# Optimization experiments

Measured on AMD Instinct MI355X. Metric: run time of the kernel, lower is better.

## Reference

```python
import jax, jax.numpy as jnp
import numpy as np

U, I, E = 50000, 100000, 1600000
D, H, HID, B = 64, 8, 8, 16384
ALPHA = 0.2  # leaky relu slope


def setup_inputs() -> dict:
    key = jax.random.key(0)
    ks = jax.random.split(key, 12)
    return {
        "userIdx": jax.random.randint(ks[0], (B,), 0, U),
        "itemIdx": jax.random.randint(ks[1], (B,), 0, I),
        "edge_u": jax.random.randint(ks[2], (E,), 0, U),
        "edge_i": jax.random.randint(ks[3], (E,), 0, I),
        "uEmbd": jax.random.normal(ks[4], (U, D), dtype=jnp.float32) * 0.01,
        "iEmbd": jax.random.normal(ks[5], (I, D), dtype=jnp.float32) * 0.01,
        "Wu_h": jax.random.normal(ks[6], (H, D, HID), dtype=jnp.float32) * 0.18,
        "Wi_h": jax.random.normal(ks[7], (H, D, HID), dtype=jnp.float32) * 0.18,
        "a_h": jax.random.normal(ks[8], (H, 2 * HID), dtype=jnp.float32) * 0.3,
        "Wu_out": jax.random.normal(ks[9], (H * HID, D), dtype=jnp.float32) * 0.15,
        "Wi_out": jax.random.normal(ks[10], (H * HID, D), dtype=jnp.float32) * 0.15,
        "a_out": jax.random.normal(ks[11], (2 * D,), dtype=jnp.float32) * 0.1,
    }


def _leaky(x):
    return jnp.where(x >= 0, x, ALPHA * x)


def _gat_layer(fu, fi, Wu, Wi, a, edge_u, edge_i):
    # fu:[U,in], fi:[I,in], Wu/Wi:[in,out], a:[2*out]
    u_h = fu @ Wu  # [U,out]
    i_h = fi @ Wi  # [I,out]
    out = Wu.shape[1]
    # a . cat(u_h[eu], i_h[ei]) decomposed into per-node scores then edge gather
    su = u_h @ a[:out]  # [U]
    si = i_h @ a[out:]  # [I]
    e = jnp.exp(-_leaky(su[edge_u] + si[edge_i]))  # [E]
    rowsum = jax.ops.segment_sum(e, edge_u, num_segments=U)  # [U]
    colsum = jax.ops.segment_sum(e, edge_i, num_segments=I)  # [I]
    # users aggregate items they interacted with
    agg_i = jax.ops.segment_sum(e[:, None] * i_h[edge_i], edge_u, num_segments=U)  # [U,out]
    u_p = u_h + agg_i / jnp.where(rowsum == 0, 1.0, rowsum)[:, None]
    # items aggregate users (nan from empty cols -> 0, as in original)
    agg_u = jax.ops.segment_sum(e[:, None] * u_h[edge_u], edge_i, num_segments=I)  # [I,out]
    att_u = jnp.where((colsum > 0)[:, None], agg_u / jnp.where(colsum == 0, 1.0, colsum)[:, None], 0.0)
    i_p = i_h + att_u
    return u_p, i_p


def reference(userIdx, itemIdx, edge_u, edge_i, uEmbd, iEmbd, Wu_h, Wi_h, a_h, Wu_out, Wi_out, a_out):
    # eval mode: all dropout layers are identity
    fu, fi = uEmbd, iEmbd
    head = jax.vmap(lambda Wu, Wi, a: _gat_layer(fu, fi, Wu, Wi, a, edge_u, edge_i))
    u_ps, i_ps = head(Wu_h, Wi_h, a_h)  # [H,U,HID], [H,I,HID]
    # concat=True heads: elu then concatenate along feature dim (head-major columns)
    hu = jax.nn.elu(u_ps).transpose(1, 0, 2).reshape(U, H * HID)
    hi = jax.nn.elu(i_ps).transpose(1, 0, 2).reshape(I, H * HID)
    u_p, i_p = _gat_layer(hu, hi, Wu_out, Wi_out, a_out, edge_u, edge_i)
    u_f = jax.nn.elu(u_p)  # final F.elu in SpUIGAT
    i_f = jax.nn.elu(i_p)
    return jnp.sum(u_f[userIdx] * i_f[itemIdx], axis=1)  # [B]
```

## Files before the change

kernel.cpp:

```cpp
#include <hip/hip_runtime.h>
#include <hip/hip_fp16.h>

#define U_N 50000
#define I_N 100000
#define E_N 1600000
#define B_N 16384
#define UI_N (U_N + I_N)
#define NB_U 782
#define NB_I 1563
#define NBK 586
#define CAP 10240
#define NBLD 512
#define CHUNK (E_N / NBLD)
#define COL_CAP 3300000
#define MAXACT 32768
#define FP8_SCALE 128.0f

typedef float f32x2 __attribute__((ext_vector_type(2)));

__global__ __launch_bounds__(1024) void k_build1(
    const int* __restrict__ eu, const int* __restrict__ ei,
    int* __restrict__ bcnt, int* __restrict__ storage) {
  __shared__ int hist[NBK];
  __shared__ int lbase[NBK];
  __shared__ int loff[NBK];
  int t = threadIdx.x;
  for (int b = t; b < NBK; b += 1024) { hist[b] = 0; loff[b] = 0; }
  __syncthreads();
  int e0 = blockIdx.x * CHUNK;
  int myu[4], myi[4];
  int ne = 0;
#pragma unroll
  for (int k = 0; k < 4; k++) {
    int e = e0 + t + 1024 * k;
    if (e < e0 + CHUNK) {
      int u = eu[e], it = ei[e];
      myu[k] = u;
      myi[k] = it;
      ne = k + 1;
      atomicAdd(&hist[u >> 8], 1);
      atomicAdd(&hist[(U_N + it) >> 8], 1);
    }
  }
  __syncthreads();
  for (int b = t; b < NBK; b += 1024) {
    int h = hist[b];
    lbase[b] = h ? atomicAdd(&bcnt[b], h) : 0;
  }
  __syncthreads();
#pragma unroll
  for (int k = 0; k < 4; k++) {
    if (k < ne) {
      int u = myu[k], it = myi[k];
      int k2 = U_N + it;
      int b1 = u >> 8;
      int s1 = lbase[b1] + atomicAdd(&loff[b1], 1);
      storage[(size_t)b1 * CAP + s1] = ((u & 255) << 18) | k2;
      int b2 = k2 >> 8;
      int s2 = lbase[b2] + atomicAdd(&loff[b2], 1);
      storage[(size_t)b2 * CAP + s2] = ((k2 & 255) << 18) | u;
    }
  }
}

__device__ void build2_body(int b, const int* __restrict__ bcnt,
                            const int* __restrict__ storage,
                            int* __restrict__ ptr, int* __restrict__ col,
                            int* smem) {
  int* c = smem;
  int* sc = smem + 256;
  int* pb = smem + 512;
  int* cur = smem + 768;
  int t = threadIdx.x;
  int pre = 0;
  for (int i = t; i < b; i += 256) pre += bcnt[i];
  sc[t] = pre;
  c[t] = 0;
  __syncthreads();
  for (int o = 128; o > 0; o >>= 1) {
    if (t < o) sc[t] += sc[t + o];
    __syncthreads();
  }
  int base = sc[0];
  __syncthreads();
  int n = bcnt[b];
  const int* s = storage + (size_t)b * CAP;
  for (int i = t; i < n; i += 256) atomicAdd(&c[s[i] >> 18], 1);
  __syncthreads();
  int deg = c[t];
  sc[t] = deg;
  __syncthreads();
  int val = deg;
  for (int o = 1; o < 256; o <<= 1) {
    int x = (t >= o) ? sc[t - o] : 0;
    __syncthreads();
    val += x;
    sc[t] = val;
    __syncthreads();
  }
  int myPtr = base + (val - deg);
  pb[t] = myPtr;
  cur[t] = 0;
  int node = b * 256 + t;
  if (node < UI_N) ptr[node] = myPtr;
  if (b == NBK - 1 && t == 255) ptr[UI_N] = base + val;
  __syncthreads();
  for (int i = t; i < n; i += 256) {
    int e = s[i];
    int local = e >> 18;
    int slot = pb[local] + atomicAdd(&cur[local], 1);
    col[slot] = e & 0x3FFFF;
  }
}

__device__ __forceinline__ void flagc_body(int bid, const int* __restrict__ uIdx,
                                           const int* __restrict__ iIdx,
                                           int* __restrict__ flag, int* __restrict__ list,
                                           int* __restrict__ nm) {
  int b = bid * 256 + threadIdx.x;
  if (b < B_N) {
    int u = uIdx[b];
    if (atomicExch(&flag[u], 1) == 0) list[atomicAdd(nm, 1)] = u;
    int it = U_N + iIdx[b];
    if (atomicExch(&flag[it], 1) == 0) list[atomicAdd(nm, 1)] = it;
  }
}

__device__ __forceinline__ void mm2_body(
    int bid, const float* __restrict__ Xu32, const float* __restrict__ Xi32,
    const __half* __restrict__ X16,
    const float* __restrict__ Wu, const float* __restrict__ Wi,
    const float* __restrict__ a, int layer,
    __half* __restrict__ f16,
    unsigned char* __restrict__ f8,
    __half* __restrict__ s16,
    float* Wl, float* Xs) {
  const bool isU = bid < NB_U;
  const int N = isU ? U_N : I_N;
  const int base = (isU ? bid : bid - NB_U) * 64;
  const int gofs = isU ? 0 : U_N;
  const float* W = isU ? Wu : Wi;
  const int aoff = (layer == 1) ? (isU ? 0 : 8) : (isU ? 0 : 64);
  int t = threadIdx.x;

  if (layer == 1) {
#pragma unroll
    for (int k = 0; k < 4; k++) {
      int i = t + 256 * k;
      int h = i >> 7, d = (i >> 1) & 63, half = i & 1;
      float4 v = *(const float4*)(W + h * 512 + d * 8 + half * 4);
      *(float4*)(Wl + d * 64 + h * 8 + half * 4) = v;
    }
    const float* X = isU ? Xu32 : Xi32;
#pragma unroll
    for (int k = 0; k < 4; k++) {
      int i = t + 256 * k;
      int r = i >> 4, ch = i & 15;
      int node = base + r;
      float4 v = make_float4(0.f, 0.f, 0.f, 0.f);
      if (node < N) v = *(const float4*)(X + (size_t)node * 64 + ch * 4);
      *(float4*)(Xs + r * 64 + ch * 4) = v;
    }
  } else {
#pragma unroll
    for (int k = 0; k < 4; k++) {
      int i = t + 256 * k;
      *(float4*)(Wl + i * 4) = *(const float4*)(W + i * 4);
    }
#pragma unroll
    for (int k = 0; k < 4; k++) {
      int i = t + 256 * k;
      int r = i >> 4, ch = i & 15;
      int node = base + r;
      float4 v = make_float4(0.f, 0.f, 0.f, 0.f);
      if (node < N) {
        const __half2* hp = (const __half2*)(X16 + (size_t)(gofs + node) * 64 + ch * 4);
        float2 f0 = __half22float2(hp[0]);
        float2 f1 = __half22float2(hp[1]);
        v = make_float4(f0.x, f0.y, f1.x, f1.y);
      }
      *(float4*)(Xs + r * 64 + ch * 4) = v;
    }
  }
  __syncthreads();

  const int c0 = t & 31;
  const int rb = t >> 5;
  float acc0[8], acc1[8];
#pragma unroll
  for (int k = 0; k < 8; k++) { acc0[k] = 0.f; acc1[k] = 0.f; }

  for (int d0 = 0; d0 < 64; d0 += 4) {
    float2 wA = *(float2*)(Wl + (d0 + 0) * 64 + 2 * c0);
    float2 wB = *(float2*)(Wl + (d0 + 1) * 64 + 2 * c0);
    float2 wC = *(float2*)(Wl + (d0 + 2) * 64 + 2 * c0);
    float2 wD = *(float2*)(Wl + (d0 + 3) * 64 + 2 * c0);
#pragma unroll
    for (int k = 0; k < 8; k++) {
      float4 x = *(float4*)(Xs + (rb + 8 * k) * 64 + d0);
      acc0[k] += x.x * wA.x + x.y * wB.x + x.z * wC.x + x.w * wD.x;
      acc1[k] += x.x * wA.y + x.y * wB.y + x.z * wC.y + x.w * wD.y;
    }
  }

  float av0, av1;
  if (layer == 1) {
    int h = c0 >> 2, j = 2 * (c0 & 3);
    av0 = a[h * 16 + aoff + j];
    av1 = a[h * 16 + aoff + j + 1];
  } else {
    av0 = a[aoff + 2 * c0];
    av1 = a[aoff + 2 * c0 + 1];
  }
#pragma unroll
  for (int k = 0; k < 8; k++) {
    int node = base + rb + 8 * k;
    float s = acc0[k] * av0 + acc1[k] * av1;
    s += __shfl_xor(s, 1);
    s += __shfl_xor(s, 2);
    if (layer != 1) {
      s += __shfl_xor(s, 4);
      s += __shfl_xor(s, 8);
      s += __shfl_xor(s, 16);
    }
    if (node < N) {
      int gn = gofs + node;
      float2 f;
      f.x = acc0[k];
      f.y = acc1[k];
      *(__half2*)(f16 + (size_t)gn * 64 + 2 * c0) = __float22half2_rn(f);
      int pk = __builtin_amdgcn_cvt_pk_fp8_f32(acc0[k] * FP8_SCALE,
                                               acc1[k] * FP8_SCALE, 0, false);
      *(unsigned short*)(f8 + (size_t)gn * 64 + 2 * c0) = (unsigned short)pk;
      if (layer == 1) {
        if ((c0 & 3) == 0) s16[gn * 8 + (c0 >> 2)] = __float2half_rn(s);
      } else {
        if (c0 == 0) s16[gn] = __float2half_rn(s);
      }
    }
  }
}

__global__ __launch_bounds__(256) void k_fused2(
    const int* __restrict__ bcnt, const int* __restrict__ storage,
    int* __restrict__ ptr, int* __restrict__ col,
    const int* __restrict__ uIdx, const int* __restrict__ iIdx,
    int* __restrict__ flag, int* __restrict__ list, int* __restrict__ nm,
    const float* __restrict__ uEmbd, const float* __restrict__ iEmbd,
    const float* __restrict__ Wu, const float* __restrict__ Wi,
    const float* __restrict__ a, __half* __restrict__ fA,
    unsigned char* __restrict__ fA8, __half* __restrict__ s16) {
  __shared__ float4 smv[2048];
  int bx = blockIdx.x;
  if (bx < NBK) {
    build2_body(bx, bcnt, storage, ptr, col, (int*)smv);
  } else if (bx < NBK + 64) {
    flagc_body(bx - NBK, uIdx, iIdx, flag, list, nm);
  } else {
    float* s = (float*)smv;
    mm2_body(bx - NBK - 64, uEmbd, iEmbd, nullptr, Wu, Wi, a, 1, fA, fA8, s16,
             s, s + 4096);
  }
}

__global__ __launch_bounds__(256) void k_mm2(
    const __half* __restrict__ X16, const float* __restrict__ Wu,
    const float* __restrict__ Wi, const float* __restrict__ a,
    __half* __restrict__ f16, unsigned char* __restrict__ f8,
    __half* __restrict__ s2) {
  __shared__ float4 smv[2048];
  float* s = (float*)smv;
  mm2_body(blockIdx.x, nullptr, nullptr, X16, Wu, Wi, a, 2, f16, f8, s2, s, s + 4096);
}

template <int LAYER>
__device__ __forceinline__ void agg_body(
    const int* __restrict__ ptr, const int* __restrict__ col,
    const unsigned char* __restrict__ f8,
    const __half* __restrict__ fA,
    __half* __restrict__ fB,
    const __half* __restrict__ sc,
    const int* __restrict__ list, const int* __restrict__ nm) {
  int gid = blockIdx.x * blockDim.x + threadIdx.x;
  int wv = gid >> 6;
  int l = threadIdx.x & 63;
  int half = l >> 5;
  int idx = wv * 2 + half;
  bool act = true;
  int n;
  if (LAYER == 2) {
    act = idx < *nm;
    n = act ? list[idx] : 0;
  } else {
    n = idx;
  }
  int lh = l & 31;
  int g = lh >> 3;
  int cc = lh & 7;

  int beg = ptr[n], endA = ptr[n + 1];
  int deg = act ? (endA - beg) : 0;
  unsigned coff = ((unsigned)(beg + g)) << 2;
  const unsigned begb = (unsigned)beg << 2;
  const unsigned f8sh = (unsigned)cc << 3;
  const unsigned ssh = (LAYER == 1) ? ((unsigned)cc << 1) : 0u;
  float sself = (LAYER == 1) ? __half2float(sc[(size_t)n * 8 + cc])
                             : __half2float(sc[n]);
  f32x2 acc2[4];
#pragma unroll
  for (int k = 0; k < 4; k++) acc2[k] = (f32x2){0.f, 0.f};
  float wsum = 0.f;
  const char* colc = (const char*)col;
  const char* f8c = (const char*)f8;
  const char* scc = (const char*)sc;

  auto edge = [&](unsigned off) {
    int nb = *(const int*)(colc + off);
    unsigned so = (LAYER == 1) ? (((unsigned)nb << 4) + ssh) : ((unsigned)nb << 1);
    float x = sself + __half2float(*(const __half*)(scc + so));
    int2 r = *(const int2*)(f8c + (((unsigned)nb << 6) + f8sh));
    float w = __expf(-fmaxf(x, 0.2f * x));
    wsum += w;
    f32x2 w2 = {w, w};
    acc2[0] += w2 * __builtin_amdgcn_cvt_pk_f32_fp8((unsigned)r.x, false);
    acc2[1] += w2 * __builtin_amdgcn_cvt_pk_f32_fp8((unsigned)r.x, true);
    acc2[2] += w2 * __builtin_amdgcn_cvt_pk_f32_fp8((unsigned)r.y, false);
    acc2[3] += w2 * __builtin_amdgcn_cvt_pk_f32_fp8((unsigned)r.y, true);
  };
  auto edgem = [&](unsigned off, bool valid) {
    unsigned o = valid ? off : begb;
    int nb = *(const int*)(colc + o);
    unsigned so = (LAYER == 1) ? (((unsigned)nb << 4) + ssh) : ((unsigned)nb << 1);
    float x = sself + __half2float(*(const __half*)(scc + so));
    int2 r = *(const int2*)(f8c + (((unsigned)nb << 6) + f8sh));
    float w = valid ? __expf(-fmaxf(x, 0.2f * x)) : 0.f;
    wsum += w;
    f32x2 w2 = {w, w};
    acc2[0] += w2 * __builtin_amdgcn_cvt_pk_f32_fp8((unsigned)r.x, false);
    acc2[1] += w2 * __builtin_amdgcn_cvt_pk_f32_fp8((unsigned)r.x, true);
    acc2[2] += w2 * __builtin_amdgcn_cvt_pk_f32_fp8((unsigned)r.y, false);
    acc2[3] += w2 * __builtin_amdgcn_cvt_pk_f32_fp8((unsigned)r.y, true);
  };

  int q = deg >> 4;
  for (; q > 0; q--) {
    edge(coff);
    edge(coff + 16);
    edge(coff + 32);
    edge(coff + 48);
    coff += 64;
  }
  int rem = deg & 15;
  if (rem) {
    edgem(coff, g < rem);
    edgem(coff + 16, (4 + g) < rem);
    if (rem > 8) {
      edgem(coff + 32, (8 + g) < rem);
      edgem(coff + 48, (12 + g) < rem);
    }
  }

#pragma unroll
  for (int k = 0; k < 4; k++) {
    f32x2 t;
    t.x = __shfl_xor(acc2[k].x, 8);
    t.y = __shfl_xor(acc2[k].y, 8);
    acc2[k] += t;
    t.x = __shfl_xor(acc2[k].x, 16);
    t.y = __shfl_xor(acc2[k].y, 16);
    acc2[k] += t;
  }
  wsum += __shfl_xor(wsum, 8);
  wsum += __shfl_xor(wsum, 16);

  if (act) {
    float inv = (deg > 0) ? 1.f / (wsum * FP8_SCALE) : 0.f;
    f32x2 a2;
    if (g == 0) a2 = acc2[0];
    else if (g == 1) a2 = acc2[1];
    else if (g == 2) a2 = acc2[2];
    else a2 = acc2[3];
    size_t boff = (size_t)n * 64 + cc * 8 + 2 * g;
    float2 sf = __half22float2(*(const __half2*)(fA + boff));
    float v0 = sf.x + a2.x * inv;
    float v1 = sf.y + a2.y * inv;
    v0 = (v0 > 0.f) ? v0 : (__expf(v0) - 1.f);
    v1 = (v1 > 0.f) ? v1 : (__expf(v1) - 1.f);
    *(__half2*)(fB + boff) = __floats2half2_rn(v0, v1);
  }
}

__global__ __launch_bounds__(256) void k_aggL1(
    const int* __restrict__ ptr, const int* __restrict__ col,
    const unsigned char* __restrict__ f8, const __half* __restrict__ fA,
    __half* __restrict__ fB, const __half* __restrict__ s16) {
  agg_body<1>(ptr, col, f8, fA, fB, s16, nullptr, nullptr);
}

__global__ __launch_bounds__(256) void k_aggL2(
    const int* __restrict__ ptr, const int* __restrict__ col,
    const unsigned char* __restrict__ f8, const __half* __restrict__ fA,
    __half* __restrict__ fB, const __half* __restrict__ s2,
    const int* __restrict__ list, const int* __restrict__ nm) {
  agg_body<2>(ptr, col, f8, fA, fB, s2, list, nm);
}

__global__ void k_dot(const int* __restrict__ uIdx, const int* __restrict__ iIdx,
                      const __half* __restrict__ u_f, const __half* __restrict__ i_f,
                      float* __restrict__ out) {
  int t = threadIdx.x;
  int pair = blockIdx.x * 32 + (t >> 3);
  int cc = t & 7;
  float4 ra = *(const float4*)(u_f + (size_t)uIdx[pair] * 64 + cc * 8);
  float4 rb = *(const float4*)(i_f + (size_t)iIdx[pair] * 64 + cc * 8);
  const __half* ha = (const __half*)&ra;
  const __half* hb = (const __half*)&rb;
  float v = 0.f;
#pragma unroll
  for (int k = 0; k < 8; k++) v += (float)ha[k] * (float)hb[k];
  v += __shfl_xor(v, 1);
  v += __shfl_xor(v, 2);
  v += __shfl_xor(v, 4);
  if (cc == 0) out[pair] = v;
}

extern "C" void kernel_launch(void* const* d_in, const int* in_sizes, int n_in,
                              void* d_out, int out_size, void* d_ws, size_t ws_size,
                              hipStream_t stream) {
  const int* userIdx = (const int*)d_in[0];
  const int* itemIdx = (const int*)d_in[1];
  const int* edge_u = (const int*)d_in[2];
  const int* edge_i = (const int*)d_in[3];
  const float* uEmbd = (const float*)d_in[4];
  const float* iEmbd = (const float*)d_in[5];
  const float* Wu_h = (const float*)d_in[6];
  const float* Wi_h = (const float*)d_in[7];
  const float* a_h = (const float*)d_in[8];
  const float* Wu_out = (const float*)d_in[9];
  const float* Wi_out = (const float*)d_in[10];
  const float* a_out = (const float*)d_in[11];
  float* out = (float*)d_out;

  char* w = (char*)d_ws;
  size_t off = 0;
  auto alloc = [&](size_t bytes) -> void* {
    void* p = w + off;
    off += (bytes + 511) & ~(size_t)511;
    return p;
  };
  int* bcnt = (int*)alloc((size_t)(NBK + 16 + UI_N) * 4);
  int* nm = bcnt + NBK;
  int* flag = bcnt + NBK + 16;
  int* ptr = (int*)alloc((size_t)(UI_N + 1) * 4);
  int* list = (int*)alloc((size_t)MAXACT * 4);
  int* col = (int*)alloc((size_t)COL_CAP * 4);
  __half* fA = (__half*)alloc((size_t)UI_N * 64 * 2);
  unsigned char* fA8 = (unsigned char*)alloc((size_t)UI_N * 64);
  __half* s16 = (__half*)alloc((size_t)UI_N * 8 * 2);
  __half* s2 = (__half*)alloc((size_t)UI_N * 2);
  size_t union_off = off;
  int* storage = (int*)alloc((size_t)NBK * CAP * 4);
  size_t end_storage = off;
  off = union_off;
  __half* fB = (__half*)alloc((size_t)UI_N * 64 * 2);
  if (off < end_storage) off = end_storage;

  hipMemsetAsync(bcnt, 0, (size_t)(NBK + 16 + UI_N) * 4, stream);
  k_build1<<<NBLD, 1024, 0, stream>>>(edge_u, edge_i, bcnt, storage);

  k_fused2<<<NBK + 64 + NB_U + NB_I, 256, 0, stream>>>(
      bcnt, storage, ptr, col, userIdx, itemIdx, flag, list, nm,
      uEmbd, iEmbd, Wu_h, Wi_h, a_h, fA, fA8, s16);

  k_aggL1<<<UI_N * 32 / 256, 256, 0, stream>>>(ptr, col, fA8, fA, fB, s16);

  k_mm2<<<NB_U + NB_I, 256, 0, stream>>>(fB, Wu_out, Wi_out, a_out, fA, fA8, s2);
  k_aggL2<<<MAXACT * 32 / 256, 256, 0, stream>>>(ptr, col, fA8, fA, fB, s2, list, nm);

  k_dot<<<B_N / 32, 256, 0, stream>>>(userIdx, itemIdx, fB, fB + (size_t)U_N * 64, out);
}
```

Before: 275.7 us.

## Stage CSR build through shared memory and skip unneeded layer-2 fp16 writes

The first build pass now counting-sorts each block's edges into LDS with 16-aligned bucket segments, then writes them to global storage in coalesced runs padded with -1. This replaces scattered per-edge global stores. The second pass skips the padding, scatters columns into LDS, and copies them out coalesced using separate true edge counts. Layer-2 matmul only writes fp16 features for flagged (queried) nodes, which cuts write traffic. The cost is larger LDS footprints that lower occupancy, fewer build blocks, and a bigger per-bucket capacity.

```diff
diff --git a/kernel.cpp b/kernel.cpp
--- a/kernel.cpp
+++ b/kernel.cpp
@@ -9,8 +9,8 @@
 #define NB_U 782
 #define NB_I 1563
 #define NBK 586
-#define CAP 10240
-#define NBLD 512
+#define CAP 16384
+#define NBLD 256
 #define CHUNK (E_N / NBLD)
 #define COL_CAP 3300000
 #define MAXACT 32768
@@ -20,60 +20,87 @@
 
 __global__ __launch_bounds__(1024) void k_build1(
     const int* __restrict__ eu, const int* __restrict__ ei,
-    int* __restrict__ bcnt, int* __restrict__ storage) {
+    int* __restrict__ bcnt, int* __restrict__ ecnt, int* __restrict__ storage) {
   __shared__ int hist[NBK];
-  __shared__ int lbase[NBK];
+  __shared__ int pb16[NBK];
+  __shared__ int gbase[NBK];
   __shared__ int loff[NBK];
+  __shared__ short map16[1344];
+  __shared__ int sc[1024];
+  __shared__ int sorted[21504];
   int t = threadIdx.x;
   for (int b = t; b < NBK; b += 1024) { hist[b] = 0; loff[b] = 0; }
   __syncthreads();
   int e0 = blockIdx.x * CHUNK;
-  int myu[4], myi[4];
-  int ne = 0;
-#pragma unroll
-  for (int k = 0; k < 4; k++) {
-    int e = e0 + t + 1024 * k;
-    if (e < e0 + CHUNK) {
+  int myu[7], myi[7];
+#pragma unroll
+  for (int k = 0; k < 7; k++) {
+    myu[k] = -1;
+    if (t + 1024 * k < CHUNK) {
+      int e = e0 + t + 1024 * k;
       int u = eu[e], it = ei[e];
       myu[k] = u;
       myi[k] = it;
-      ne = k + 1;
       atomicAdd(&hist[u >> 8], 1);
       atomicAdd(&hist[(U_N + it) >> 8], 1);
     }
   }
   __syncthreads();
-  for (int b = t; b < NBK; b += 1024) {
-    int h = hist[b];
-    lbase[b] = h ? atomicAdd(&bcnt[b], h) : 0;
-  }
-  __syncthreads();
-#pragma unroll
-  for (int k = 0; k < 4; k++) {
-    if (k < ne) {
+  int ph = (t < NBK) ? ((hist[t] + 15) & ~15) : 0;
+  sc[t] = ph;
+  __syncthreads();
+  int val = ph;
+  for (int o = 1; o < 1024; o <<= 1) {
+    int x = (t >= o) ? sc[t - o] : 0;
+    __syncthreads();
+    val += x;
+    sc[t] = val;
+    __syncthreads();
+  }
+  int total16 = sc[1023];
+  if (t < NBK) {
+    int myb = val - ph;
+    pb16[t] = myb;
+    gbase[t] = ph ? atomicAdd(&bcnt[t], ph) : 0;
+    if (hist[t]) atomicAdd(&ecnt[t], hist[t]);
+    for (int k = myb >> 4; k < (myb + ph) >> 4; k++) map16[k] = (short)t;
+  }
+  for (int j = t; j < total16; j += 1024) sorted[j] = -1;
+  __syncthreads();
+#pragma unroll
+  for (int k = 0; k < 7; k++) {
+    if (myu[k] >= 0) {
       int u = myu[k], it = myi[k];
       int k2 = U_N + it;
       int b1 = u >> 8;
-      int s1 = lbase[b1] + atomicAdd(&loff[b1], 1);
-      storage[(size_t)b1 * CAP + s1] = ((u & 255) << 18) | k2;
+      int p1 = pb16[b1] + atomicAdd(&loff[b1], 1);
+      sorted[p1] = ((u & 255) << 18) | k2;
       int b2 = k2 >> 8;
-      int s2 = lbase[b2] + atomicAdd(&loff[b2], 1);
-      storage[(size_t)b2 * CAP + s2] = ((k2 & 255) << 18) | u;
-    }
+      int p2 = pb16[b2] + atomicAdd(&loff[b2], 1);
+      sorted[p2] = ((k2 & 255) << 18) | u;
+    }
+  }
+  __syncthreads();
+  for (int j = t; j < total16; j += 1024) {
+    int b = map16[j >> 4];
+    storage[(size_t)b * CAP + gbase[b] + (j - pb16[b])] = sorted[j];
   }
 }
 
 __device__ void build2_body(int b, const int* __restrict__ bcnt,
+                            const int* __restrict__ ecnt,
                             const int* __restrict__ storage,
                             int* __restrict__ ptr, int* __restrict__ col,
                             int* smem) {
   int* c = smem;
   int* sc = smem + 256;
-  int* pb = smem + 512;
+  int* pbl = smem + 512;
   int* cur = smem + 768;
+  int* tot = smem + 1024;
+  int* lcol = smem + 1040;
   int t = threadIdx.x;
   int pre = 0;
-  for (int i = t; i < b; i += 256) pre += bcnt[i];
+  for (int i = t; i < b; i += 256) pre += ecnt[i];
   sc[t] = pre;
   c[t] = 0;
   __syncthreads();
@@ -85,7 +112,10 @@
   __syncthreads();
   int n = bcnt[b];
   const int* s = storage + (size_t)b * CAP;
-  for (int i = t; i < n; i += 256) atomicAdd(&c[s[i] >> 18], 1);
+  for (int i = t; i < n; i += 256) {
+    int e = s[i];
+    if (e >= 0) atomicAdd(&c[e >> 18], 1);
+  }
   __syncthreads();
   int deg = c[t];
   sc[t] = deg;
@@ -98,19 +128,25 @@
     sc[t] = val;
     __syncthreads();
   }
-  int myPtr = base + (val - deg);
-  pb[t] = myPtr;
+  int myoff = val - deg;
+  pbl[t] = myoff;
   cur[t] = 0;
+  if (t == 255) tot[0] = val;
   int node = b * 256 + t;
-  if (node < UI_N) ptr[node] = myPtr;
+  if (node < UI_N) ptr[node] = base + myoff;
   if (b == NBK - 1 && t == 255) ptr[UI_N] = base + val;
   __syncthreads();
   for (int i = t; i < n; i += 256) {
     int e = s[i];
-    int local = e >> 18;
-    int slot = pb[local] + atomicAdd(&cur[local], 1);
-    col[slot] = e & 0x3FFFF;
-  }
+    if (e >= 0) {
+      int local = e >> 18;
+      int pos = pbl[local] + atomicAdd(&cur[local], 1);
+      lcol[pos] = e & 0x3FFFF;
+    }
+  }
+  __syncthreads();
+  int vt = tot[0];
+  for (int i = t; i < vt; i += 256) col[base + i] = lcol[i];
 }
 
 __device__ __forceinline__ void flagc_body(int bid, const int* __restrict__ uIdx,
@@ -131,9 +167,8 @@
     const __half* __restrict__ X16,
     const float* __restrict__ Wu, const float* __restrict__ Wi,
     const float* __restrict__ a, int layer,
-    __half* __restrict__ f16,
-    unsigned char* __restrict__ f8,
-    __half* __restrict__ s16,
+    __half* __restrict__ f16, unsigned char* __restrict__ f8,
+    __half* __restrict__ s16, const int* __restrict__ flagp,
     float* Wl, float* Xs) {
   const bool isU = bid < NB_U;
   const int N = isU ? U_N : I_N;
@@ -225,10 +260,12 @@
     }
     if (node < N) {
       int gn = gofs + node;
-      float2 f;
-      f.x = acc0[k];
-      f.y = acc1[k];
-      *(__half2*)(f16 + (size_t)gn * 64 + 2 * c0) = __float22half2_rn(f);
+      if (layer == 1 || flagp[gn]) {
+        float2 f;
+        f.x = acc0[k];
+        f.y = acc1[k];
+        *(__half2*)(f16 + (size_t)gn * 64 + 2 * c0) = __float22half2_rn(f);
+      }
       int pk = __builtin_amdgcn_cvt_pk_fp8_f32(acc0[k] * FP8_SCALE,
                                                acc1[k] * FP8_SCALE, 0, false);
       *(unsigned short*)(f8 + (size_t)gn * 64 + 2 * c0) = (unsigned short)pk;
@@ -242,7 +279,8 @@
 }
 
 __global__ __launch_bounds__(256) void k_fused2(
-    const int* __restrict__ bcnt, const int* __restrict__ storage,
+    const int* __restrict__ bcnt, const int* __restrict__ ecnt,
+    const int* __restrict__ storage,
     int* __restrict__ ptr, int* __restrict__ col,
     const int* __restrict__ uIdx, const int* __restrict__ iIdx,
     int* __restrict__ flag, int* __restrict__ list, int* __restrict__ nm,
@@ -250,16 +288,16 @@
     const float* __restrict__ Wu, const float* __restrict__ Wi,
     const float* __restrict__ a, __half* __restrict__ fA,
     unsigned char* __restrict__ fA8, __half* __restrict__ s16) {
-  __shared__ float4 smv[2048];
+  __shared__ __align__(16) int smem_i[11296];
   int bx = blockIdx.x;
   if (bx < NBK) {
-    build2_body(bx, bcnt, storage, ptr, col, (int*)smv);
+    build2_body(bx, bcnt, ecnt, storage, ptr, col, smem_i);
   } else if (bx < NBK + 64) {
     flagc_body(bx - NBK, uIdx, iIdx, flag, list, nm);
   } else {
-    float* s = (float*)smv;
+    float* s = (float*)smem_i;
     mm2_body(bx - NBK - 64, uEmbd, iEmbd, nullptr, Wu, Wi, a, 1, fA, fA8, s16,
-             s, s + 4096);
+             nullptr, s, s + 4096);
   }
 }
 
@@ -267,10 +305,10 @@
     const __half* __restrict__ X16, const float* __restrict__ Wu,
     const float* __restrict__ Wi, const float* __restrict__ a,
     __half* __restrict__ f16, unsigned char* __restrict__ f8,
-    __half* __restrict__ s2) {
-  __shared__ float4 smv[2048];
-  float* s = (float*)smv;
-  mm2_body(blockIdx.x, nullptr, nullptr, X16, Wu, Wi, a, 2, f16, f8, s2, s, s + 4096);
+    __half* __restrict__ s2, const int* __restrict__ flag) {
+  __shared__ __align__(16) float smv[8192];
+  mm2_body(blockIdx.x, nullptr, nullptr, X16, Wu, Wi, a, 2, f16, f8, s2, flag,
+           smv, smv + 4096);
 }
 
 template <int LAYER>
@@ -448,9 +486,10 @@
     off += (bytes + 511) & ~(size_t)511;
     return p;
   };
-  int* bcnt = (int*)alloc((size_t)(NBK + 16 + UI_N) * 4);
-  int* nm = bcnt + NBK;
-  int* flag = bcnt + NBK + 16;
+  int* bcnt = (int*)alloc((size_t)(2 * NBK + 16 + UI_N) * 4);
+  int* ecnt = bcnt + NBK;
+  int* nm = bcnt + 2 * NBK;
+  int* flag = bcnt + 2 * NBK + 16;
   int* ptr = (int*)alloc((size_t)(UI_N + 1) * 4);
   int* list = (int*)alloc((size_t)MAXACT * 4);
   int* col = (int*)alloc((size_t)COL_CAP * 4);
@@ -465,16 +504,16 @@
   __half* fB = (__half*)alloc((size_t)UI_N * 64 * 2);
   if (off < end_storage) off = end_storage;
 
-  hipMemsetAsync(bcnt, 0, (size_t)(NBK + 16 + UI_N) * 4, stream);
-  k_build1<<<NBLD, 1024, 0, stream>>>(edge_u, edge_i, bcnt, storage);
+  hipMemsetAsync(bcnt, 0, (size_t)(2 * NBK + 16 + UI_N) * 4, stream);
+  k_build1<<<NBLD, 1024, 0, stream>>>(edge_u, edge_i, bcnt, ecnt, storage);
 
   k_fused2<<<NBK + 64 + NB_U + NB_I, 256, 0, stream>>>(
-      bcnt, storage, ptr, col, userIdx, itemIdx, flag, list, nm,
+      bcnt, ecnt, storage, ptr, col, userIdx, itemIdx, flag, list, nm,
       uEmbd, iEmbd, Wu_h, Wi_h, a_h, fA, fA8, s16);
 
   k_aggL1<<<UI_N * 32 / 256, 256, 0, stream>>>(ptr, col, fA8, fA, fB, s16);
 
-  k_mm2<<<NB_U + NB_I, 256, 0, stream>>>(fB, Wu_out, Wi_out, a_out, fA, fA8, s2);
+  k_mm2<<<NB_U + NB_I, 256, 0, stream>>>(fB, Wu_out, Wi_out, a_out, fA, fA8, s2, flag);
   k_aggL2<<<MAXACT * 32 / 256, 256, 0, stream>>>(ptr, col, fA8, fA, fB, s2, list, nm);
 
   k_dot<<<B_N / 32, 256, 0, stream>>>(userIdx, itemIdx, fB, fB + (size_t)U_N * 64, out);
```

Result: no change. 270.4 us (-1.9%).

## Replace bucketed CSR build with global degree count, scan, and atomic scatter

Applied to the files above, without the earlier changes.

The two-pass bucket-storage CSR build is replaced by three steps: a per-node degree count with global atomics, a per-256-node prefix-scan kernel, and a scatter that claims slots with global atomicAdd cursors. The scatter runs in the same launch as the layer-1 projection. This drops the large intermediate storage buffer and its extra read and write pass, but adds an extra kernel launch and heavy global atomic contention on per-node counters. Two smaller changes ride along: attention scores are pre-multiplied by log2(e) so the edge weight uses exp2f instead of __expf, and layer 2 writes fp16 features only for flagged nodes.

```diff
diff --git a/kernel.cpp b/kernel.cpp
--- a/kernel.cpp
+++ b/kernel.cpp
@@ -9,109 +9,14 @@
 #define NB_U 782
 #define NB_I 1563
 #define NBK 586
-#define CAP 10240
-#define NBLD 512
-#define CHUNK (E_N / NBLD)
+#define NCB 2000
+#define ECB 800
 #define COL_CAP 3300000
 #define MAXACT 32768
 #define FP8_SCALE 128.0f
+#define LOG2E 1.44269504088896f
 
 typedef float f32x2 __attribute__((ext_vector_type(2)));
-
-__global__ __launch_bounds__(1024) void k_build1(
-    const int* __restrict__ eu, const int* __restrict__ ei,
-    int* __restrict__ bcnt, int* __restrict__ storage) {
-  __shared__ int hist[NBK];
-  __shared__ int lbase[NBK];
-  __shared__ int loff[NBK];
-  int t = threadIdx.x;
-  for (int b = t; b < NBK; b += 1024) { hist[b] = 0; loff[b] = 0; }
-  __syncthreads();
-  int e0 = blockIdx.x * CHUNK;
-  int myu[4], myi[4];
-  int ne = 0;
-#pragma unroll
-  for (int k = 0; k < 4; k++) {
-    int e = e0 + t + 1024 * k;
-    if (e < e0 + CHUNK) {
-      int u = eu[e], it = ei[e];
-      myu[k] = u;
-      myi[k] = it;
-      ne = k + 1;
-      atomicAdd(&hist[u >> 8], 1);
-      atomicAdd(&hist[(U_N + it) >> 8], 1);
-    }
-  }
-  __syncthreads();
-  for (int b = t; b < NBK; b += 1024) {
-    int h = hist[b];
-    lbase[b] = h ? atomicAdd(&bcnt[b], h) : 0;
-  }
-  __syncthreads();
-#pragma unroll
-  for (int k = 0; k < 4; k++) {
-    if (k < ne) {
-      int u = myu[k], it = myi[k];
-      int k2 = U_N + it;
-      int b1 = u >> 8;
-      int s1 = lbase[b1] + atomicAdd(&loff[b1], 1);
-      storage[(size_t)b1 * CAP + s1] = ((u & 255) << 18) | k2;
-      int b2 = k2 >> 8;
-      int s2 = lbase[b2] + atomicAdd(&loff[b2], 1);
-      storage[(size_t)b2 * CAP + s2] = ((k2 & 255) << 18) | u;
-    }
-  }
-}
-
-__device__ void build2_body(int b, const int* __restrict__ bcnt,
-                            const int* __restrict__ storage,
-                            int* __restrict__ ptr, int* __restrict__ col,
-                            int* smem) {
-  int* c = smem;
-  int* sc = smem + 256;
-  int* pb = smem + 512;
-  int* cur = smem + 768;
-  int t = threadIdx.x;
-  int pre = 0;
-  for (int i = t; i < b; i += 256) pre += bcnt[i];
-  sc[t] = pre;
-  c[t] = 0;
-  __syncthreads();
-  for (int o = 128; o > 0; o >>= 1) {
-    if (t < o) sc[t] += sc[t + o];
-    __syncthreads();
-  }
-  int base = sc[0];
-  __syncthreads();
-  int n = bcnt[b];
-  const int* s = storage + (size_t)b * CAP;
-  for (int i = t; i < n; i += 256) atomicAdd(&c[s[i] >> 18], 1);
-  __syncthreads();
-  int deg = c[t];
-  sc[t] = deg;
-  __syncthreads();
-  int val = deg;
-  for (int o = 1; o < 256; o <<= 1) {
-    int x = (t >= o) ? sc[t - o] : 0;
-    __syncthreads();
-    val += x;
-    sc[t] = val;
-    __syncthreads();
-  }
-  int myPtr = base + (val - deg);
-  pb[t] = myPtr;
-  cur[t] = 0;
-  int node = b * 256 + t;
-  if (node < UI_N) ptr[node] = myPtr;
-  if (b == NBK - 1 && t == 255) ptr[UI_N] = base + val;
-  __syncthreads();
-  for (int i = t; i < n; i += 256) {
-    int e = s[i];
-    int local = e >> 18;
-    int slot = pb[local] + atomicAdd(&cur[local], 1);
-    col[slot] = e & 0x3FFFF;
-  }
-}
 
 __device__ __forceinline__ void flagc_body(int bid, const int* __restrict__ uIdx,
                                            const int* __restrict__ iIdx,
@@ -126,14 +31,79 @@
   }
 }
 
+__global__ __launch_bounds__(256) void k_count(
+    const int* __restrict__ eu, const int* __restrict__ ei,
+    const int* __restrict__ uIdx, const int* __restrict__ iIdx,
+    int* __restrict__ deg, int* __restrict__ bsum,
+    int* __restrict__ flag, int* __restrict__ list, int* __restrict__ nm) {
+  int bx = blockIdx.x;
+  int t = threadIdx.x;
+  if (bx < NCB) {
+    __shared__ int hist[NBK];
+    for (int b = t; b < NBK; b += 256) hist[b] = 0;
+    __syncthreads();
+    int e0 = bx * ECB;
+#pragma unroll
+    for (int k = 0; k < 4; k++) {
+      if (t + 256 * k < ECB) {
+        int e = e0 + t + 256 * k;
+        int u = eu[e], it = ei[e];
+        atomicAdd(&deg[u], 1);
+        atomicAdd(&deg[U_N + it], 1);
+        atomicAdd(&hist[u >> 8], 1);
+        atomicAdd(&hist[(U_N + it) >> 8], 1);
+      }
+    }
+    __syncthreads();
+    for (int b = t; b < NBK; b += 256)
+      if (hist[b]) atomicAdd(&bsum[b], hist[b]);
+  } else {
+    flagc_body(bx - NCB, uIdx, iIdx, flag, list, nm);
+  }
+}
+
+__global__ __launch_bounds__(256) void k_ptr(
+    const int* __restrict__ deg, const int* __restrict__ bsum,
+    int* __restrict__ ptr, int* __restrict__ gcur) {
+  __shared__ int sc[256];
+  int b = blockIdx.x, t = threadIdx.x;
+  int pre = 0;
+  for (int i = t; i < b; i += 256) pre += bsum[i];
+  sc[t] = pre;
+  __syncthreads();
+  for (int o = 128; o > 0; o >>= 1) {
+    if (t < o) sc[t] += sc[t + o];
+    __syncthreads();
+  }
+  int base = sc[0];
+  __syncthreads();
+  int node = b * 256 + t;
+  int d = (node < UI_N) ? deg[node] : 0;
+  sc[t] = d;
+  __syncthreads();
+  int val = d;
+  for (int o = 1; o < 256; o <<= 1) {
+    int x = (t >= o) ? sc[t - o] : 0;
+    __syncthreads();
+    val += x;
+    sc[t] = val;
+    __syncthreads();
+  }
+  int myPtr = base + val - d;
+  if (node < UI_N) {
+    ptr[node] = myPtr;
+    gcur[node] = myPtr;
+  }
+  if (b == NBK - 1 && t == 255) ptr[UI_N] = base + val;
+}
+
 __device__ __forceinline__ void mm2_body(
     int bid, const float* __restrict__ Xu32, const float* __restrict__ Xi32,
     const __half* __restrict__ X16,
     const float* __restrict__ Wu, const float* __restrict__ Wi,
     const float* __restrict__ a, int layer,
-    __half* __restrict__ f16,
-    unsigned char* __restrict__ f8,
-    __half* __restrict__ s16,
+    __half* __restrict__ f16, unsigned char* __restrict__ f8,
+    __half* __restrict__ s16, const int* __restrict__ flagp,
     float* Wl, float* Xs) {
   const bool isU = bid < NB_U;
   const int N = isU ? U_N : I_N;
@@ -225,41 +195,50 @@
     }
     if (node < N) {
       int gn = gofs + node;
-      float2 f;
-      f.x = acc0[k];
-      f.y = acc1[k];
-      *(__half2*)(f16 + (size_t)gn * 64 + 2 * c0) = __float22half2_rn(f);
+      if (layer == 1 || flagp[gn]) {
+        float2 f;
+        f.x = acc0[k];
+        f.y = acc1[k];
+        *(__half2*)(f16 + (size_t)gn * 64 + 2 * c0) = __float22half2_rn(f);
+      }
       int pk = __builtin_amdgcn_cvt_pk_fp8_f32(acc0[k] * FP8_SCALE,
                                                acc1[k] * FP8_SCALE, 0, false);
       *(unsigned short*)(f8 + (size_t)gn * 64 + 2 * c0) = (unsigned short)pk;
       if (layer == 1) {
-        if ((c0 & 3) == 0) s16[gn * 8 + (c0 >> 2)] = __float2half_rn(s);
+        if ((c0 & 3) == 0) s16[gn * 8 + (c0 >> 2)] = __float2half_rn(s * LOG2E);
       } else {
-        if (c0 == 0) s16[gn] = __float2half_rn(s);
+        if (c0 == 0) s16[gn] = __float2half_rn(s * LOG2E);
       }
     }
   }
 }
 
-__global__ __launch_bounds__(256) void k_fused2(
-    const int* __restrict__ bcnt, const int* __restrict__ storage,
-    int* __restrict__ ptr, int* __restrict__ col,
-    const int* __restrict__ uIdx, const int* __restrict__ iIdx,
-    int* __restrict__ flag, int* __restrict__ list, int* __restrict__ nm,
+__global__ __launch_bounds__(256) void k_fusedS(
+    const int* __restrict__ eu, const int* __restrict__ ei,
+    int* __restrict__ gcur, int* __restrict__ col,
     const float* __restrict__ uEmbd, const float* __restrict__ iEmbd,
     const float* __restrict__ Wu, const float* __restrict__ Wi,
     const float* __restrict__ a, __half* __restrict__ fA,
     unsigned char* __restrict__ fA8, __half* __restrict__ s16) {
-  __shared__ float4 smv[2048];
+  __shared__ __align__(16) float smv[8192];
   int bx = blockIdx.x;
-  if (bx < NBK) {
-    build2_body(bx, bcnt, storage, ptr, col, (int*)smv);
-  } else if (bx < NBK + 64) {
-    flagc_body(bx - NBK, uIdx, iIdx, flag, list, nm);
+  int t = threadIdx.x;
+  if (bx < NCB) {
+    int e0 = bx * ECB;
+#pragma unroll
+    for (int k = 0; k < 4; k++) {
+      if (t + 256 * k < ECB) {
+        int e = e0 + t + 256 * k;
+        int u = eu[e], it = ei[e];
+        int p1 = atomicAdd(&gcur[u], 1);
+        col[p1] = U_N + it;
+        int p2 = atomicAdd(&gcur[U_N + it], 1);
+        col[p2] = u;
+      }
+    }
   } else {
-    float* s = (float*)smv;
-    mm2_body(bx - NBK - 64, uEmbd, iEmbd, nullptr, Wu, Wi, a, 1, fA, fA8, s16,
-             s, s + 4096);
+    mm2_body(bx - NCB, uEmbd, iEmbd, nullptr, Wu, Wi, a, 1, fA, fA8, s16,
+             nullptr, smv, smv + 4096);
   }
 }
 
@@ -267,10 +246,10 @@
     const __half* __restrict__ X16, const float* __restrict__ Wu,
     const float* __restrict__ Wi, const float* __restrict__ a,
     __half* __restrict__ f16, unsigned char* __restrict__ f8,
-    __half* __restrict__ s2) {
-  __shared__ float4 smv[2048];
-  float* s = (float*)smv;
-  mm2_body(blockIdx.x, nullptr, nullptr, X16, Wu, Wi, a, 2, f16, f8, s2, s, s + 4096);
+    __half* __restrict__ s2, const int* __restrict__ flag) {
+  __shared__ __align__(16) float smv[8192];
+  mm2_body(blockIdx.x, nullptr, nullptr, X16, Wu, Wi, a, 2, f16, f8, s2, flag,
+           smv, smv + 4096);
 }
 
 template <int LAYER>
@@ -319,7 +298,7 @@
     unsigned so = (LAYER == 1) ? (((unsigned)nb << 4) + ssh) : ((unsigned)nb << 1);
     float x = sself + __half2float(*(const __half*)(scc + so));
     int2 r = *(const int2*)(f8c + (((unsigned)nb << 6) + f8sh));
-    float w = __expf(-fmaxf(x, 0.2f * x));
+    float w = exp2f(-fmaxf(x, 0.2f * x));
     wsum += w;
     f32x2 w2 = {w, w};
     acc2[0] += w2 * __builtin_amdgcn_cvt_pk_f32_fp8((unsigned)r.x, false);
@@ -333,7 +312,7 @@
     unsigned so = (LAYER == 1) ? (((unsigned)nb << 4) + ssh) : ((unsigned)nb << 1);
     float x = sself + __half2float(*(const __half*)(scc + so));
     int2 r = *(const int2*)(f8c + (((unsigned)nb << 6) + f8sh));
-    float w = valid ? __expf(-fmaxf(x, 0.2f * x)) : 0.f;
+    float w = valid ? exp2f(-fmaxf(x, 0.2f * x)) : 0.f;
     wsum += w;
     f32x2 w2 = {w, w};
     acc2[0] += w2 * __builtin_amdgcn_cvt_pk_f32_fp8((unsigned)r.x, false);
@@ -448,33 +427,32 @@
     off += (bytes + 511) & ~(size_t)511;
     return p;
   };
-  int* bcnt = (int*)alloc((size_t)(NBK + 16 + UI_N) * 4);
-  int* nm = bcnt + NBK;
-  int* flag = bcnt + NBK + 16;
+  int* bsum = (int*)alloc((size_t)(NBK + 16 + 2 * UI_N) * 4);
+  int* nm = bsum + NBK;
+  int* flag = bsum + NBK + 16;
+  int* deg = bsum + NBK + 16 + UI_N;
   int* ptr = (int*)alloc((size_t)(UI_N + 1) * 4);
+  int* gcur = (int*)alloc((size_t)UI_N * 4);
   int* list = (int*)alloc((size_t)MAXACT * 4);
   int* col = (int*)alloc((size_t)COL_CAP * 4);
   __half* fA = (__half*)alloc((size_t)UI_N * 64 * 2);
   unsigned char* fA8 = (unsigned char*)alloc((size_t)UI_N * 64);
   __half* s16 = (__half*)alloc((size_t)UI_N * 8 * 2);
   __half* s2 = (__half*)alloc((size_t)UI_N * 2);
-  size_t union_off = off;
-  int* storage = (int*)alloc((size_t)NBK * CAP * 4);
-  size_t end_storage = off;
-  off = union_off;
   __half* fB = (__half*)alloc((size_t)UI_N * 64 * 2);
-  if (off < end_storage) off = end_storage;
-
-  hipMemsetAsync(bcnt, 0, (size_t)(NBK + 16 + UI_N) * 4, stream);
-  k_build1<<<NBLD, 1024, 0, stream>>>(edge_u, edge_i, bcnt, storage);
-
-  k_fused2<<<NBK + 64 + NB_U + NB_I, 256, 0, stream>>>(
-      bcnt, storage, ptr, col, userIdx, itemIdx, flag, list, nm,
-      uEmbd, iEmbd, Wu_h, Wi_h, a_h, fA, fA8, s16);
+
+  hipMemsetAsync(bsum, 0, (size_t)(NBK + 16 + 2 * UI_N) * 4, stream);
+
+  k_count<<<NCB + B_N / 256, 256, 0, stream>>>(edge_u, edge_i, userIdx, itemIdx,
+                                               deg, bsum, flag, list, nm);
+  k_ptr<<<NBK, 256, 0, stream>>>(deg, bsum, ptr, gcur);
+  k_fusedS<<<NCB + NB_U + NB_I, 256, 0, stream>>>(edge_u, edge_i, gcur, col,
+                                                  uEmbd, iEmbd, Wu_h, Wi_h, a_h,
+                                                  fA, fA8, s16);
 
   k_aggL1<<<UI_N * 32 / 256, 256, 0, stream>>>(ptr, col, fA8, fA, fB, s16);
 
-  k_mm2<<<NB_U + NB_I, 256, 0, stream>>>(fB, Wu_out, Wi_out, a_out, fA, fA8, s2);
+  k_mm2<<<NB_U + NB_I, 256, 0, stream>>>(fB, Wu_out, Wi_out, a_out, fA, fA8, s2, flag);
   k_aggL2<<<MAXACT * 32 / 256, 256, 0, stream>>>(ptr, col, fA8, fA, fB, s2, list, nm);
 
   k_dot<<<B_N / 32, 256, 0, stream>>>(userIdx, itemIdx, fB, fB + (size_t)U_N * 64, out);
```

New measurement: 699.8 us. 2.54x slower.
